# Performance work log

Measured on AMD Instinct MI355X. Metric: run time of the kernel, lower is better.

## Reference

```python
import jax, jax.numpy as jnp
import numpy as np

N_NODES = 100000


def setup_inputs() -> dict:
    key = jax.random.key(0)
    ks = jax.random.split(key, 8)
    IN, HID, OUT = 128, 128, 64
    E = 1600000
    x = jax.random.normal(ks[0], (N_NODES, IN), dtype=jnp.float32)
    edge_index = jax.random.randint(ks[1], (2, E), 0, N_NODES, dtype=jnp.int64)
    # PyG SAGEConv params: lin_l (applied to aggregated neighbors, with bias),
    # lin_r (root weight, no bias).
    def lin(k, fi, fo):
        return jax.random.normal(k, (fi, fo), dtype=jnp.float32) / np.sqrt(fi)
    Wl0 = lin(ks[2], IN, HID)
    bl0 = jnp.zeros((HID,), dtype=jnp.float32)
    Wr0 = lin(ks[3], IN, HID)
    Wl1 = lin(ks[4], HID, OUT)
    bl1 = jnp.zeros((OUT,), dtype=jnp.float32)
    Wr1 = lin(ks[5], HID, OUT)
    return {"x": x, "edge_index": edge_index,
            "Wl0": Wl0, "bl0": bl0, "Wr0": Wr0,
            "Wl1": Wl1, "bl1": bl1, "Wr1": Wr1}


def _sage_conv(h, src, dst, Wl, bl, Wr):
    # mean aggregation of source features onto target nodes
    summed = jax.ops.segment_sum(h[src], dst, num_segments=N_NODES)  # [N, d]
    cnt = jax.ops.segment_sum(jnp.ones((src.shape[0], 1), h.dtype), dst,
                              num_segments=N_NODES)                  # [N, 1]
    agg = summed / jnp.maximum(cnt, 1.0)
    return agg @ Wl + bl + h @ Wr


def reference(x, edge_index, Wl0, bl0, Wr0, Wl1, bl1, Wr1):
    src, dst = edge_index[0], edge_index[1]
    h = jax.nn.relu(_sage_conv(x, src, dst, Wl0, bl0, Wr0))
    # dropout is identity in eval mode (training=False)
    return _sage_conv(h, src, dst, Wl1, bl1, Wr1)
```

## Files before the change

### kernel.cpp

```cpp
#include <hip/hip_runtime.h>


typedef short short8 __attribute__((ext_vector_type(8)));
typedef float f32x4 __attribute__((ext_vector_type(4)));
typedef float f32x2 __attribute__((ext_vector_type(2)));

#define NBUCK 782
#define BCAP  3072
#define EPB   8192

static __device__ __forceinline__ unsigned short f2bf(float f) {
    union { float f; unsigned u; } c; c.f = f;
    unsigned u = c.u + 0x7fffu + ((c.u >> 16) & 1u);
    return (unsigned short)(u >> 16);
}
static __device__ __forceinline__ float bf2f(unsigned short b) {
    union { unsigned u; float f; } c; c.u = ((unsigned)b) << 16;
    return c.f;
}
static __device__ __forceinline__ float bf2f_s(short b) {
    return bf2f((unsigned short)b);
}

static __device__ __forceinline__ unsigned char f2fp8(float x) {
    union { float f; unsigned u; } c; c.f = x;
    unsigned s = (c.u >> 24) & 0x80u;
    float a = __builtin_fabsf(x);
    if (a < 0.015625f) {
        int m = (int)rintf(a * 512.0f);
        return (unsigned char)(s | (unsigned)m);
    }
    unsigned u = c.u + 0x7ffffu + ((c.u >> 20) & 1u);
    int e = (int)((u >> 23) & 0xff) - 120;
    unsigned m = (u >> 20) & 7u;
    if (e > 15) { e = 15; m = 6; }
    return (unsigned char)(s | (unsigned)(e << 3) | m);
}

static __device__ __forceinline__ void acc_fp8x4(unsigned w, float* a) {
#if __has_builtin(__builtin_amdgcn_cvt_pk_f32_fp8)
    f32x2 lo = __builtin_amdgcn_cvt_pk_f32_fp8((int)w, false);
    f32x2 hi = __builtin_amdgcn_cvt_pk_f32_fp8((int)w, true);
    a[0] += lo[0]; a[1] += lo[1]; a[2] += hi[0]; a[3] += hi[1];
#else
    #pragma unroll
    for (int j = 0; j < 4; ++j) {
        unsigned b = (w >> (8 * j)) & 0xffu;
        union { unsigned u; float f; } c;
        c.u = ((b & 0x80u) << 24) | ((b & 0x7fu) << 20);
        a[j] += c.f * 0x1p120f;
    }
#endif
}
static __device__ __forceinline__ void acc_row16(uint4 w, float* a) {
    acc_fp8x4(w.x, a + 0);  acc_fp8x4(w.y, a + 4);
    acc_fp8x4(w.z, a + 8);  acc_fp8x4(w.w, a + 12);
}

__global__ __launch_bounds__(256) void k_pack2(const float* __restrict__ Wl0,
        const float* __restrict__ Wr0, const float* __restrict__ Wl1,
        const float* __restrict__ Wr1, unsigned short* __restrict__ Wp0,
        unsigned short* __restrict__ Wp1) {
    int tid = blockIdx.x * 256 + threadIdx.x;
    const float *WA, *WB; int CA; unsigned short* Wp;
    if (tid < 4096) {
        WA = Wl0; WB = Wr0; CA = 128; Wp = Wp0;
    } else {
        tid -= 4096;
        if (tid >= 2048) return;
        WA = Wl1; WB = Wr1; CA = 64; Wp = Wp1;
    }
    int lane = tid & 63, kk = (tid >> 6) & 3, tg = tid >> 8;
    int l15 = lane & 15, quad = lane >> 4;
    int c = tg * 16 + l15;
    const float* W = (c < CA) ? WA : WB;
    int cc = (c < CA) ? c : c - CA;
    short8 v;
    #pragma unroll
    for (int j = 0; j < 8; ++j) {
        int k = kk * 32 + quad * 8 + j;
        v[j] = (short)f2bf(W[(size_t)k * CA + cc]);
    }
    *(short8*)(Wp + (size_t)tid * 8) = v;
}

__global__ __launch_bounds__(256) void k_gemm0_bucket(
        const float* __restrict__ X, const unsigned short* __restrict__ Wp,
        unsigned char* __restrict__ P0, unsigned short* __restrict__ Q0, int Nrows,
        const int* __restrict__ src, const int* __restrict__ dst,
        int* __restrict__ cursor, int* __restrict__ bregion,
        int E, int bucketBlocks) {
    const int t = threadIdx.x;
    if ((int)blockIdx.x >= bucketBlocks) {
        const int wave = t >> 6, lane = t & 63;
        const int quad = lane >> 4, l15 = lane & 15;
        const int row0 = (blockIdx.x - bucketBlocks) * 32;
        const int c0w = wave * 64;
        float4 xf[4][2][2];
        #pragma unroll
        for (int mt = 0; mt < 2; ++mt) {
            int row = row0 + mt * 16 + l15;
            if (row > Nrows - 1) row = Nrows - 1;
            const float* xp = X + (size_t)row * 128 + quad * 8;
            #pragma unroll
            for (int kk = 0; kk < 4; ++kk) {
                xf[kk][mt][0] = *(const float4*)(xp + kk * 32);
                xf[kk][mt][1] = *(const float4*)(xp + kk * 32 + 4);
            }
        }
        short8 a[4][2];
        #pragma unroll
        for (int kk = 0; kk < 4; ++kk)
            #pragma unroll
            for (int mt = 0; mt < 2; ++mt) {
                float4 f0 = xf[kk][mt][0], f1 = xf[kk][mt][1];
                short8 v;
                v[0] = (short)f2bf(f0.x); v[1] = (short)f2bf(f0.y);
                v[2] = (short)f2bf(f0.z); v[3] = (short)f2bf(f0.w);
                v[4] = (short)f2bf(f1.x); v[5] = (short)f2bf(f1.y);
                v[6] = (short)f2bf(f1.z); v[7] = (short)f2bf(f1.w);
                a[kk][mt] = v;
            }
        f32x4 acc[2][4];
        #pragma unroll
        for (int mt = 0; mt < 2; ++mt)
            #pragma unroll
            for (int tt = 0; tt < 4; ++tt) acc[mt][tt] = (f32x4){0.f, 0.f, 0.f, 0.f};
        #pragma unroll
        for (int kk = 0; kk < 4; ++kk) {
            short8 b[4];
            #pragma unroll
            for (int tt = 0; tt < 4; ++tt) {
                int tg = (c0w >> 4) + tt;
                b[tt] = *(const short8*)(Wp + ((size_t)(tg * 4 + kk) * 64 + lane) * 8);
            }
            #pragma unroll
            for (int mt = 0; mt < 2; ++mt)
                #pragma unroll
                for (int tt = 0; tt < 4; ++tt)
                    acc[mt][tt] = __builtin_amdgcn_mfma_f32_16x16x32_bf16(
                        a[kk][mt], b[tt], acc[mt][tt], 0, 0, 0);
        }
        #pragma unroll
        for (int mt = 0; mt < 2; ++mt)
            #pragma unroll
            for (int r = 0; r < 4; ++r) {
                int row = row0 + mt * 16 + quad * 4 + r;
                if (row < Nrows) {
                    if (c0w < 128) {
                        #pragma unroll
                        for (int tt = 0; tt < 4; ++tt)
                            P0[(size_t)row * 128 + c0w + tt * 16 + l15] =
                                f2fp8(acc[mt][tt][r]);
                    } else {
                        #pragma unroll
                        for (int tt = 0; tt < 4; ++tt)
                            Q0[(size_t)row * 128 + (c0w - 128) + tt * 16 + l15] =
                                f2bf(acc[mt][tt][r]);
                    }
                }
            }
        return;
    }
    __shared__ int hist[NBUCK];
    __shared__ int basel[NBUCK];
    int bid = blockIdx.x;
    for (int i = t; i < NBUCK; i += 256) hist[i] = 0;
    __syncthreads();
    int e0 = bid * EPB + t * 32;
    if (e0 + 32 <= E) {
        #pragma unroll
        for (int q = 0; q < 8; ++q) {
            int4 v = *(const int4*)(dst + e0 + q * 4);
            atomicAdd(&hist[v.x >> 7], 1);
            atomicAdd(&hist[v.y >> 7], 1);
            atomicAdd(&hist[v.z >> 7], 1);
            atomicAdd(&hist[v.w >> 7], 1);
        }
    } else {
        for (int j = 0; j < 32; ++j)
            if (e0 + j < E) atomicAdd(&hist[dst[e0 + j] >> 7], 1);
    }
    __syncthreads();
    for (int i = t; i < NBUCK; i += 256) {
        int c = hist[i];
        basel[i] = (c > 0) ? atomicAdd(&cursor[i], c) : 0;
    }
    __syncthreads();
    for (int i = t; i < NBUCK; i += 256) hist[i] = 0;
    __syncthreads();
    if (e0 + 32 <= E) {
        #pragma unroll
        for (int q = 0; q < 8; ++q) {
            int4 dv = *(const int4*)(dst + e0 + q * 4);
            int4 sv = *(const int4*)(src + e0 + q * 4);
            int dd[4] = {dv.x, dv.y, dv.z, dv.w};
            int ss[4] = {sv.x, sv.y, sv.z, sv.w};
            #pragma unroll
            for (int j = 0; j < 4; ++j) {
                int b = dd[j] >> 7;
                int r = atomicAdd(&hist[b], 1);
                bregion[(size_t)b * BCAP + basel[b] + r] = ss[j] | ((dd[j] & 127) << 20);
            }
        }
    } else {
        for (int j = 0; j < 32; ++j) {
            if (e0 + j < E) {
                int dd = dst[e0 + j], ss = src[e0 + j];
                int b = dd >> 7;
                int r = atomicAdd(&hist[b], 1);
                bregion[(size_t)b * BCAP + basel[b] + r] = ss | ((dd & 127) << 20);
            }
        }
    }
}

__global__ __launch_bounds__(256) void k_csr(const int* __restrict__ cursor,
                                             const int* __restrict__ bregion,
                                             int* __restrict__ rowptr,
                                             int* __restrict__ csr, int Nn) {
    __shared__ int words[BCAP];
    __shared__ int hist[128], sc[128], rank[128];
    __shared__ int red[256];
    int b = blockIdx.x, t = threadIdx.x;
    int part = 0;
    for (int i = t; i < b; i += 256) part += cursor[i];
    red[t] = part;
    if (t < 128) { hist[t] = 0; rank[t] = 0; }
    __syncthreads();
    #pragma unroll
    for (int off = 128; off > 0; off >>= 1) {
        if (t < off) red[t] += red[t + off];
        __syncthreads();
    }
    int gbase = red[0];
    int cnt = cursor[b];
    for (int i = t; i < cnt; i += 256) {
        int w = bregion[(size_t)b * BCAP + i];
        words[i] = w;
        atomicAdd(&hist[w >> 20], 1);
    }
    __syncthreads();
    if (t < 128) sc[t] = hist[t];
    __syncthreads();
    #pragma unroll
    for (int off = 1; off < 128; off <<= 1) {
        int x = 0;
        if (t < 128 && t >= off) x = sc[t - off];
        __syncthreads();
        if (t < 128) sc[t] += x;
        __syncthreads();
    }
    if (t < 128) sc[t] -= hist[t];
    __syncthreads();
    if (t < 128) {
        int node = b * 128 + t;
        if (node <= Nn) rowptr[node] = gbase + sc[t];
    }
    for (int i = t; i < cnt; i += 256) {
        int w = words[i];
        int d7 = w >> 20;
        int r = atomicAdd(&rank[d7], 1);
        csr[gbase + sc[d7] + r] = w & 0xFFFFF;
    }
}

__global__ __launch_bounds__(256) void k_agg0_gemm1(
        const unsigned char* __restrict__ P0,
        const unsigned short* __restrict__ Q0,
        const int* __restrict__ rowptr, const int* __restrict__ csr,
        const float* __restrict__ bl0,
        const unsigned short* __restrict__ Wp,
        unsigned char* __restrict__ P1, unsigned short* __restrict__ Q1,
        int Nn) {
    __shared__ unsigned short ht[32 * 128];
    const int t = threadIdx.x;
    const int wave = t >> 6, lane = t & 63;
    {
        int g = lane >> 3, l7 = lane & 7;
        int nloc = wave * 8 + g;
        int n = blockIdx.x * 32 + nloc;
        bool live = (n < Nn);
        int st = 0, dg = 0;
        if (live) { st = rowptr[n]; dg = rowptr[n + 1] - st; }
        float acc[16] = {};
        int e = 0;
        for (; e + 2 <= dg; e += 2) {
            int s0 = csr[st + e];
            int s1 = csr[st + e + 1];
            uint4 w0 = *(const uint4*)(P0 + (size_t)s0 * 128 + l7 * 16);
            uint4 w1 = *(const uint4*)(P0 + (size_t)s1 * 128 + l7 * 16);
            acc_row16(w0, acc);
            acc_row16(w1, acc);
        }
        if (e < dg) {
            int s0 = csr[st + e];
            uint4 w0 = *(const uint4*)(P0 + (size_t)s0 * 128 + l7 * 16);
            acc_row16(w0, acc);
        }
        short8 o0 = (short8){0,0,0,0,0,0,0,0}, o1 = o0;
        if (live) {
            float inv = 1.f / fmaxf((float)dg, 1.f);
            short8 q0 = *(const short8*)(Q0 + (size_t)n * 128 + l7 * 16);
            short8 q1 = *(const short8*)(Q0 + (size_t)n * 128 + l7 * 16 + 8);
            float bb[16];
            *(float4*)(bb + 0)  = *(const float4*)(bl0 + l7 * 16);
            *(float4*)(bb + 4)  = *(const float4*)(bl0 + l7 * 16 + 4);
            *(float4*)(bb + 8)  = *(const float4*)(bl0 + l7 * 16 + 8);
            *(float4*)(bb + 12) = *(const float4*)(bl0 + l7 * 16 + 12);
            #pragma unroll
            for (int j = 0; j < 8; ++j)
                o0[j] = (short)f2bf(fmaxf(acc[j] * inv + bb[j] + bf2f_s(q0[j]), 0.f));
            #pragma unroll
            for (int j = 0; j < 8; ++j)
                o1[j] = (short)f2bf(fmaxf(acc[8 + j] * inv + bb[8 + j] + bf2f_s(q1[j]), 0.f));
        }
        unsigned sw = (unsigned)(nloc & 7) << 4;
        char* base = (char*)ht + nloc * 256;
        *(short8*)(base + (((unsigned)(l7 * 32)) ^ sw)) = o0;
        *(short8*)(base + (((unsigned)(l7 * 32 + 16)) ^ sw)) = o1;
    }
    __syncthreads();
    const int quad = lane >> 4, l15 = lane & 15;
    const int row0 = blockIdx.x * 32;
    const int c0w = wave * 32;
    f32x4 acc[2][2];
    #pragma unroll
    for (int mt = 0; mt < 2; ++mt)
        #pragma unroll
        for (int tt = 0; tt < 2; ++tt) acc[mt][tt] = (f32x4){0.f, 0.f, 0.f, 0.f};
    #pragma unroll
    for (int kk = 0; kk < 4; ++kk) {
        short8 a[2];
        #pragma unroll
        for (int mt = 0; mt < 2; ++mt) {
            int row = mt * 16 + l15;
            const char* p = (const char*)ht + row * 256 +
                (((unsigned)(kk * 64 + quad * 16)) ^ ((unsigned)(row & 7) << 4));
            a[mt] = *(const short8*)p;
        }
        short8 b[2];
        #pragma unroll
        for (int tt = 0; tt < 2; ++tt) {
            int tg = (c0w >> 4) + tt;
            b[tt] = *(const short8*)(Wp + ((size_t)(tg * 4 + kk) * 64 + lane) * 8);
        }
        #pragma unroll
        for (int mt = 0; mt < 2; ++mt)
            #pragma unroll
            for (int tt = 0; tt < 2; ++tt)
                acc[mt][tt] = __builtin_amdgcn_mfma_f32_16x16x32_bf16(
                    a[mt], b[tt], acc[mt][tt], 0, 0, 0);
    }
    #pragma unroll
    for (int mt = 0; mt < 2; ++mt)
        #pragma unroll
        for (int r = 0; r < 4; ++r) {
            int row = row0 + mt * 16 + quad * 4 + r;
            if (row < Nn) {
                if (c0w < 64) {
                    #pragma unroll
                    for (int tt = 0; tt < 2; ++tt)
                        P1[(size_t)row * 64 + c0w + tt * 16 + l15] =
                            f2fp8(acc[mt][tt][r]);
                } else {
                    #pragma unroll
                    for (int tt = 0; tt < 2; ++tt)
                        Q1[(size_t)row * 64 + (c0w - 64) + tt * 16 + l15] =
                            f2bf(acc[mt][tt][r]);
                }
            }
        }
}

__global__ __launch_bounds__(256) void k_agg1(const unsigned char* __restrict__ P1,
                                              const unsigned short* __restrict__ Q1,
                                              const int* __restrict__ rowptr,
                                              const int* __restrict__ csr,
                                              const float* __restrict__ bl1,
                                              float* __restrict__ out, int Nn) {
    int wave = threadIdx.x >> 6, lane = threadIdx.x & 63;
    int g = lane >> 2, l3 = lane & 3;
    int n = (blockIdx.x * 4 + wave) * 16 + g;
    bool live = (n < Nn);
    int st = 0, dg = 0;
    if (live) { st = rowptr[n]; dg = rowptr[n + 1] - st; }
    float acc[16] = {};
    int e = 0;
    for (; e + 2 <= dg; e += 2) {
        int s0 = csr[st + e];
        int s1 = csr[st + e + 1];
        uint4 w0 = *(const uint4*)(P1 + (size_t)s0 * 64 + l3 * 16);
        uint4 w1 = *(const uint4*)(P1 + (size_t)s1 * 64 + l3 * 16);
        acc_row16(w0, acc);
        acc_row16(w1, acc);
    }
    if (e < dg) {
        int s0 = csr[st + e];
        uint4 w0 = *(const uint4*)(P1 + (size_t)s0 * 64 + l3 * 16);
        acc_row16(w0, acc);
    }
    if (live) {
        float inv = 1.f / fmaxf((float)dg, 1.f);
        short8 q0 = *(const short8*)(Q1 + (size_t)n * 64 + l3 * 16);
        short8 q1 = *(const short8*)(Q1 + (size_t)n * 64 + l3 * 16 + 8);
        float bb[16];
        *(float4*)(bb + 0)  = *(const float4*)(bl1 + l3 * 16);
        *(float4*)(bb + 4)  = *(const float4*)(bl1 + l3 * 16 + 4);
        *(float4*)(bb + 8)  = *(const float4*)(bl1 + l3 * 16 + 8);
        *(float4*)(bb + 12) = *(const float4*)(bl1 + l3 * 16 + 12);
        float4 o[4];
        #pragma unroll
        for (int j = 0; j < 8; ++j)
            ((float*)o)[j] = acc[j] * inv + bb[j] + bf2f_s(q0[j]);
        #pragma unroll
        for (int j = 0; j < 8; ++j)
            ((float*)o)[8 + j] = acc[8 + j] * inv + bb[8 + j] + bf2f_s(q1[j]);
        #pragma unroll
        for (int q = 0; q < 4; ++q)
            *(float4*)(out + (size_t)n * 64 + l3 * 16 + q * 4) = o[q];
    }
}

extern "C" void kernel_launch(void* const* d_in, const int* in_sizes, int n_in,
                              void* d_out, int out_size, void* d_ws, size_t ws_size,
                              hipStream_t stream) {
    const float* x   = (const float*)d_in[0];
    const int* eidx  = (const int*)d_in[1];
    const float* Wl0 = (const float*)d_in[2];
    const float* bl0 = (const float*)d_in[3];
    const float* Wr0 = (const float*)d_in[4];
    const float* Wl1 = (const float*)d_in[5];
    const float* bl1 = (const float*)d_in[6];
    const float* Wr1 = (const float*)d_in[7];
    float* out = (float*)d_out;

    const int N = in_sizes[0] / 128;
    const int E = in_sizes[1] / 2;
    const int* src = eidx;
    const int* dst = eidx + E;

    int* rowptr  = (int*)d_ws;
    int* cursor  = rowptr + (N + 4);
    int* bregion = cursor + 784;
    int* csr     = bregion + (size_t)NBUCK * BCAP;
    unsigned short* Wp0 = (unsigned short*)(csr + E);
    unsigned short* Wp1 = Wp0 + 32768;
    unsigned char*  P0  = (unsigned char*)(Wp1 + 16384);
    unsigned short* Q0  = (unsigned short*)(P0 + (size_t)N * 128);
    unsigned char*  P1  = (unsigned char*)(Q0 + (size_t)N * 128);
    unsigned short* Q1  = (unsigned short*)(P1 + (size_t)N * 64);

    hipMemsetAsync(cursor, 0, NBUCK * sizeof(int), stream);

    k_pack2<<<24, 256, 0, stream>>>(Wl0, Wr0, Wl1, Wr1, Wp0, Wp1);

    int gemmBlocks = (N + 31) / 32;
    int nbb = (E + EPB - 1) / EPB;
    k_gemm0_bucket<<<gemmBlocks + nbb, 256, 0, stream>>>(
        x, Wp0, P0, Q0, N, src, dst, cursor, bregion, E, nbb);
    k_csr<<<NBUCK, 256, 0, stream>>>(cursor, bregion, rowptr, csr, N);

    k_agg0_gemm1<<<(N + 31) / 32, 256, 0, stream>>>(
        P0, Q0, rowptr, csr, bl0, Wp1, P1, Q1, N);
    k_agg1<<<(N + 63) / 64, 256, 0, stream>>>(P1, Q1, rowptr, csr, bl1, out, N);
}
```

Measured before the change: 278.6 us.

## Split bucket and gemm0 kernels; stage bucketed edges in LDS for coalesced writes

The fused gemm0+bucket kernel is split into two separate launches, k_bucket and k_gemm0. The bucketing kernel now scans the per-block histogram to sort its edges locally in shared memory, then writes them to the bucket regions in bucket order rather than scattering single words. This aims to make global writes contiguous per bucket. In exchange, the bucket kernel uses much more LDS (about 56KB), which lowers its occupancy, and it adds an extra launch plus a serialized stage that can no longer overlap with the GEMM blocks.

```diff
diff --git a/kernel.cpp b/kernel.cpp
--- a/kernel.cpp
+++ b/kernel.cpp
@@ -84,87 +84,17 @@
     *(short8*)(Wp + (size_t)tid * 8) = v;
 }
 
-__global__ __launch_bounds__(256) void k_gemm0_bucket(
-        const float* __restrict__ X, const unsigned short* __restrict__ Wp,
-        unsigned char* __restrict__ P0, unsigned short* __restrict__ Q0, int Nrows,
+__global__ __launch_bounds__(256) void k_bucket(
         const int* __restrict__ src, const int* __restrict__ dst,
-        int* __restrict__ cursor, int* __restrict__ bregion,
-        int E, int bucketBlocks) {
+        int* __restrict__ cursor, int* __restrict__ bregion, int E) {
+    __shared__ int hist[NBUCK];
+    __shared__ int obase[NBUCK];
+    __shared__ int basel[NBUCK];
+    __shared__ int stagedw[EPB];
+    __shared__ unsigned short stagedb[EPB];
+    __shared__ int scanred[256];
     const int t = threadIdx.x;
-    if ((int)blockIdx.x >= bucketBlocks) {
-        const int wave = t >> 6, lane = t & 63;
-        const int quad = lane >> 4, l15 = lane & 15;
-        const int row0 = (blockIdx.x - bucketBlocks) * 32;
-        const int c0w = wave * 64;
-        float4 xf[4][2][2];
-        #pragma unroll
-        for (int mt = 0; mt < 2; ++mt) {
-            int row = row0 + mt * 16 + l15;
-            if (row > Nrows - 1) row = Nrows - 1;
-            const float* xp = X + (size_t)row * 128 + quad * 8;
-            #pragma unroll
-            for (int kk = 0; kk < 4; ++kk) {
-                xf[kk][mt][0] = *(const float4*)(xp + kk * 32);
-                xf[kk][mt][1] = *(const float4*)(xp + kk * 32 + 4);
-            }
-        }
-        short8 a[4][2];
-        #pragma unroll
-        for (int kk = 0; kk < 4; ++kk)
-            #pragma unroll
-            for (int mt = 0; mt < 2; ++mt) {
-                float4 f0 = xf[kk][mt][0], f1 = xf[kk][mt][1];
-                short8 v;
-                v[0] = (short)f2bf(f0.x); v[1] = (short)f2bf(f0.y);
-                v[2] = (short)f2bf(f0.z); v[3] = (short)f2bf(f0.w);
-                v[4] = (short)f2bf(f1.x); v[5] = (short)f2bf(f1.y);
-                v[6] = (short)f2bf(f1.z); v[7] = (short)f2bf(f1.w);
-                a[kk][mt] = v;
-            }
-        f32x4 acc[2][4];
-        #pragma unroll
-        for (int mt = 0; mt < 2; ++mt)
-            #pragma unroll
-            for (int tt = 0; tt < 4; ++tt) acc[mt][tt] = (f32x4){0.f, 0.f, 0.f, 0.f};
-        #pragma unroll
-        for (int kk = 0; kk < 4; ++kk) {
-            short8 b[4];
-            #pragma unroll
-            for (int tt = 0; tt < 4; ++tt) {
-                int tg = (c0w >> 4) + tt;
-                b[tt] = *(const short8*)(Wp + ((size_t)(tg * 4 + kk) * 64 + lane) * 8);
-            }
-            #pragma unroll
-            for (int mt = 0; mt < 2; ++mt)
-                #pragma unroll
-                for (int tt = 0; tt < 4; ++tt)
-                    acc[mt][tt] = __builtin_amdgcn_mfma_f32_16x16x32_bf16(
-                        a[kk][mt], b[tt], acc[mt][tt], 0, 0, 0);
-        }
-        #pragma unroll
-        for (int mt = 0; mt < 2; ++mt)
-            #pragma unroll
-            for (int r = 0; r < 4; ++r) {
-                int row = row0 + mt * 16 + quad * 4 + r;
-                if (row < Nrows) {
-                    if (c0w < 128) {
-                        #pragma unroll
-                        for (int tt = 0; tt < 4; ++tt)
-                            P0[(size_t)row * 128 + c0w + tt * 16 + l15] =
-                                f2fp8(acc[mt][tt][r]);
-                    } else {
-                        #pragma unroll
-                        for (int tt = 0; tt < 4; ++tt)
-                            Q0[(size_t)row * 128 + (c0w - 128) + tt * 16 + l15] =
-                                f2bf(acc[mt][tt][r]);
-                    }
-                }
-            }
-        return;
-    }
-    __shared__ int hist[NBUCK];
-    __shared__ int basel[NBUCK];
-    int bid = blockIdx.x;
+    const int bid = blockIdx.x;
     for (int i = t; i < NBUCK; i += 256) hist[i] = 0;
     __syncthreads();
     int e0 = bid * EPB + t * 32;
@@ -182,10 +112,30 @@
             if (e0 + j < E) atomicAdd(&hist[dst[e0 + j] >> 7], 1);
     }
     __syncthreads();
-    for (int i = t; i < NBUCK; i += 256) {
-        int c = hist[i];
-        basel[i] = (c > 0) ? atomicAdd(&cursor[i], c) : 0;
-    }
+    int i0 = t * 4;
+    int h0 = (i0 + 0 < NBUCK) ? hist[i0 + 0] : 0;
+    int h1 = (i0 + 1 < NBUCK) ? hist[i0 + 1] : 0;
+    int h2 = (i0 + 2 < NBUCK) ? hist[i0 + 2] : 0;
+    int h3 = (i0 + 3 < NBUCK) ? hist[i0 + 3] : 0;
+    int lsum = h0 + h1 + h2 + h3;
+    scanred[t] = lsum;
+    __syncthreads();
+    #pragma unroll
+    for (int off = 1; off < 256; off <<= 1) {
+        int x = (t >= off) ? scanred[t - off] : 0;
+        __syncthreads();
+        scanred[t] += x;
+        __syncthreads();
+    }
+    int excl = scanred[t] - lsum;
+    if (i0 + 0 < NBUCK) obase[i0 + 0] = excl;
+    if (i0 + 1 < NBUCK) obase[i0 + 1] = excl + h0;
+    if (i0 + 2 < NBUCK) obase[i0 + 2] = excl + h0 + h1;
+    if (i0 + 3 < NBUCK) obase[i0 + 3] = excl + h0 + h1 + h2;
+    if (i0 + 0 < NBUCK) basel[i0 + 0] = h0 ? atomicAdd(&cursor[i0 + 0], h0) : 0;
+    if (i0 + 1 < NBUCK) basel[i0 + 1] = h1 ? atomicAdd(&cursor[i0 + 1], h1) : 0;
+    if (i0 + 2 < NBUCK) basel[i0 + 2] = h2 ? atomicAdd(&cursor[i0 + 2], h2) : 0;
+    if (i0 + 3 < NBUCK) basel[i0 + 3] = h3 ? atomicAdd(&cursor[i0 + 3], h3) : 0;
     __syncthreads();
     for (int i = t; i < NBUCK; i += 256) hist[i] = 0;
     __syncthreads();
@@ -200,7 +150,9 @@
             for (int j = 0; j < 4; ++j) {
                 int b = dd[j] >> 7;
                 int r = atomicAdd(&hist[b], 1);
-                bregion[(size_t)b * BCAP + basel[b] + r] = ss[j] | ((dd[j] & 127) << 20);
+                int slot = obase[b] + r;
+                stagedw[slot] = ss[j] | ((dd[j] & 127) << 20);
+                stagedb[slot] = (unsigned short)b;
             }
         }
     } else {
@@ -209,10 +161,94 @@
                 int dd = dst[e0 + j], ss = src[e0 + j];
                 int b = dd >> 7;
                 int r = atomicAdd(&hist[b], 1);
-                bregion[(size_t)b * BCAP + basel[b] + r] = ss | ((dd & 127) << 20);
+                int slot = obase[b] + r;
+                stagedw[slot] = ss | ((dd & 127) << 20);
+                stagedb[slot] = (unsigned short)b;
             }
         }
     }
+    __syncthreads();
+    int tot = E - bid * EPB; if (tot > EPB) tot = EPB;
+    for (int i = t; i < tot; i += 256) {
+        int w = stagedw[i];
+        int b = stagedb[i];
+        bregion[(size_t)b * BCAP + basel[b] + (i - obase[b])] = w;
+    }
+}
+
+__global__ __launch_bounds__(256) void k_gemm0(
+        const float* __restrict__ X, const unsigned short* __restrict__ Wp,
+        unsigned char* __restrict__ P0, unsigned short* __restrict__ Q0,
+        int Nrows) {
+    const int t = threadIdx.x;
+    const int wave = t >> 6, lane = t & 63;
+    const int quad = lane >> 4, l15 = lane & 15;
+    const int row0 = blockIdx.x * 32;
+    const int c0w = wave * 64;
+    float4 xf[4][2][2];
+    #pragma unroll
+    for (int mt = 0; mt < 2; ++mt) {
+        int row = row0 + mt * 16 + l15;
+        if (row > Nrows - 1) row = Nrows - 1;
+        const float* xp = X + (size_t)row * 128 + quad * 8;
+        #pragma unroll
+        for (int kk = 0; kk < 4; ++kk) {
+            xf[kk][mt][0] = *(const float4*)(xp + kk * 32);
+            xf[kk][mt][1] = *(const float4*)(xp + kk * 32 + 4);
+        }
+    }
+    short8 a[4][2];
+    #pragma unroll
+    for (int kk = 0; kk < 4; ++kk)
+        #pragma unroll
+        for (int mt = 0; mt < 2; ++mt) {
+            float4 f0 = xf[kk][mt][0], f1 = xf[kk][mt][1];
+            short8 v;
+            v[0] = (short)f2bf(f0.x); v[1] = (short)f2bf(f0.y);
+            v[2] = (short)f2bf(f0.z); v[3] = (short)f2bf(f0.w);
+            v[4] = (short)f2bf(f1.x); v[5] = (short)f2bf(f1.y);
+            v[6] = (short)f2bf(f1.z); v[7] = (short)f2bf(f1.w);
+            a[kk][mt] = v;
+        }
+    f32x4 acc[2][4];
+    #pragma unroll
+    for (int mt = 0; mt < 2; ++mt)
+        #pragma unroll
+        for (int tt = 0; tt < 4; ++tt) acc[mt][tt] = (f32x4){0.f, 0.f, 0.f, 0.f};
+    #pragma unroll
+    for (int kk = 0; kk < 4; ++kk) {
+        short8 b[4];
+        #pragma unroll
+        for (int tt = 0; tt < 4; ++tt) {
+            int tg = (c0w >> 4) + tt;
+            b[tt] = *(const short8*)(Wp + ((size_t)(tg * 4 + kk) * 64 + lane) * 8);
+        }
+        #pragma unroll
+        for (int mt = 0; mt < 2; ++mt)
+            #pragma unroll
+            for (int tt = 0; tt < 4; ++tt)
+                acc[mt][tt] = __builtin_amdgcn_mfma_f32_16x16x32_bf16(
+                    a[kk][mt], b[tt], acc[mt][tt], 0, 0, 0);
+    }
+    #pragma unroll
+    for (int mt = 0; mt < 2; ++mt)
+        #pragma unroll
+        for (int r = 0; r < 4; ++r) {
+            int row = row0 + mt * 16 + quad * 4 + r;
+            if (row < Nrows) {
+                if (c0w < 128) {
+                    #pragma unroll
+                    for (int tt = 0; tt < 4; ++tt)
+                        P0[(size_t)row * 128 + c0w + tt * 16 + l15] =
+                            f2fp8(acc[mt][tt][r]);
+                } else {
+                    #pragma unroll
+                    for (int tt = 0; tt < 4; ++tt)
+                        Q0[(size_t)row * 128 + (c0w - 128) + tt * 16 + l15] =
+                            f2bf(acc[mt][tt][r]);
+                }
+            }
+        }
 }
 
 __global__ __launch_bounds__(256) void k_csr(const int* __restrict__ cursor,
@@ -455,10 +491,9 @@
 
     k_pack2<<<24, 256, 0, stream>>>(Wl0, Wr0, Wl1, Wr1, Wp0, Wp1);
 
-    int gemmBlocks = (N + 31) / 32;
     int nbb = (E + EPB - 1) / EPB;
-    k_gemm0_bucket<<<gemmBlocks + nbb, 256, 0, stream>>>(
-        x, Wp0, P0, Q0, N, src, dst, cursor, bregion, E, nbb);
+    k_bucket<<<nbb, 256, 0, stream>>>(src, dst, cursor, bregion, E);
+    k_gemm0<<<(N + 31) / 32, 256, 0, stream>>>(x, Wp0, P0, Q0, N);
     k_csr<<<NBUCK, 256, 0, stream>>>(cursor, bregion, rowptr, csr, N);
 
     k_agg0_gemm1<<<(N + 31) / 32, 256, 0, stream>>>(
```

Measured after the change: 294.7 us. 5.8% more time.

## Balance neighbor aggregation by splitting block edge ranges evenly across lanes

Applied to the files above, without the earlier changes.

Both aggregation kernels now split the contiguous CSR edge range of a node block evenly across lane groups, instead of giving each group one node's edges. Each CSR word keeps the local destination index in its high bits, so a group can tell when it crosses a node boundary and flush its partial sums into a shared-memory accumulator with atomics. The goal is to remove load imbalance and divergence from uneven node degrees, and to software-pipeline the next row gather. The cost is extra LDS atomics, zero-initialisation and additional barriers.

```diff
diff --git a/kernel.cpp b/kernel.cpp
--- a/kernel.cpp
+++ b/kernel.cpp
@@ -261,7 +261,7 @@
         int w = words[i];
         int d7 = w >> 20;
         int r = atomicAdd(&rank[d7], 1);
-        csr[gbase + sc[d7] + r] = w & 0xFFFFF;
+        csr[gbase + sc[d7] + r] = w;
     }
 }
 
@@ -273,34 +273,66 @@
         const unsigned short* __restrict__ Wp,
         unsigned char* __restrict__ P1, unsigned short* __restrict__ Q1,
         int Nn) {
+    __shared__ float accs[32 * 128];
     __shared__ unsigned short ht[32 * 128];
     const int t = threadIdx.x;
     const int wave = t >> 6, lane = t & 63;
+    const int n0 = blockIdx.x * 32;
     {
-        int g = lane >> 3, l7 = lane & 7;
-        int nloc = wave * 8 + g;
-        int n = blockIdx.x * 32 + nloc;
-        bool live = (n < Nn);
-        int st = 0, dg = 0;
-        if (live) { st = rowptr[n]; dg = rowptr[n + 1] - st; }
-        float acc[16] = {};
-        int e = 0;
-        for (; e + 2 <= dg; e += 2) {
-            int s0 = csr[st + e];
-            int s1 = csr[st + e + 1];
-            uint4 w0 = *(const uint4*)(P0 + (size_t)s0 * 128 + l7 * 16);
-            uint4 w1 = *(const uint4*)(P0 + (size_t)s1 * 128 + l7 * 16);
-            acc_row16(w0, acc);
-            acc_row16(w1, acc);
-        }
-        if (e < dg) {
-            int s0 = csr[st + e];
-            uint4 w0 = *(const uint4*)(P0 + (size_t)s0 * 128 + l7 * 16);
-            acc_row16(w0, acc);
-        }
+        int l7 = lane & 7;
+        int g = wave * 8 + (lane >> 3);
+        for (int i2 = t; i2 < 32 * 128; i2 += 256) accs[i2] = 0.f;
+        __syncthreads();
+        int st0 = rowptr[n0];
+        int en  = rowptr[n0 + 32];
+        int T = en - st0;
+        int q = (T + 31) >> 5;
+        int gbeg = st0 + g * q; if (gbeg > en) gbeg = en;
+        int gend = gbeg + q;    if (gend > en) gend = en;
+        float a[16];
+        #pragma unroll
+        for (int j = 0; j < 16; ++j) a[j] = 0.f;
+        int cur = -1;
+        int i = gbeg;
+        int wcur = 0; uint4 rcur = (uint4){0, 0, 0, 0};
+        if (i < gend) {
+            wcur = csr[i];
+            rcur = *(const uint4*)(P0 + (size_t)(wcur & 0xFFFFF) * 128 + l7 * 16);
+        }
+        while (i < gend) {
+            int wnext = 0; uint4 rnext = rcur;
+            if (i + 1 < gend) {
+                wnext = csr[i + 1];
+                rnext = *(const uint4*)(P0 + (size_t)(wnext & 0xFFFFF) * 128 + l7 * 16);
+            }
+            int loc = (wcur >> 20) & 31;
+            if (loc != cur) {
+                if (cur >= 0) {
+                    #pragma unroll
+                    for (int j = 0; j < 16; ++j)
+                        atomicAdd(&accs[cur * 128 + l7 * 16 + j], a[j]);
+                    #pragma unroll
+                    for (int j = 0; j < 16; ++j) a[j] = 0.f;
+                }
+                cur = loc;
+            }
+            acc_row16(rcur, a);
+            wcur = wnext; rcur = rnext; ++i;
+        }
+        if (cur >= 0) {
+            #pragma unroll
+            for (int j = 0; j < 16; ++j)
+                atomicAdd(&accs[cur * 128 + l7 * 16 + j], a[j]);
+        }
+        __syncthreads();
+        int n = n0 + g;
         short8 o0 = (short8){0,0,0,0,0,0,0,0}, o1 = o0;
-        if (live) {
-            float inv = 1.f / fmaxf((float)dg, 1.f);
+        if (n < Nn) {
+            int dgr = rowptr[n + 1] - rowptr[n];
+            float inv = 1.f / fmaxf((float)dgr, 1.f);
+            float va[16];
+            #pragma unroll
+            for (int j = 0; j < 16; ++j) va[j] = accs[g * 128 + l7 * 16 + j];
             short8 q0 = *(const short8*)(Q0 + (size_t)n * 128 + l7 * 16);
             short8 q1 = *(const short8*)(Q0 + (size_t)n * 128 + l7 * 16 + 8);
             float bb[16];
@@ -310,13 +342,13 @@
             *(float4*)(bb + 12) = *(const float4*)(bl0 + l7 * 16 + 12);
             #pragma unroll
             for (int j = 0; j < 8; ++j)
-                o0[j] = (short)f2bf(fmaxf(acc[j] * inv + bb[j] + bf2f_s(q0[j]), 0.f));
+                o0[j] = (short)f2bf(fmaxf(va[j] * inv + bb[j] + bf2f_s(q0[j]), 0.f));
             #pragma unroll
             for (int j = 0; j < 8; ++j)
-                o1[j] = (short)f2bf(fmaxf(acc[8 + j] * inv + bb[8 + j] + bf2f_s(q1[j]), 0.f));
-        }
-        unsigned sw = (unsigned)(nloc & 7) << 4;
-        char* base = (char*)ht + nloc * 256;
+                o1[j] = (short)f2bf(fmaxf(va[8 + j] * inv + bb[8 + j] + bf2f_s(q1[j]), 0.f));
+        }
+        unsigned sw = (unsigned)(g & 7) << 4;
+        char* base = (char*)ht + g * 256;
         *(short8*)(base + (((unsigned)(l7 * 32)) ^ sw)) = o0;
         *(short8*)(base + (((unsigned)(l7 * 32 + 16)) ^ sw)) = o1;
     }
@@ -379,29 +411,64 @@
                                               const int* __restrict__ csr,
                                               const float* __restrict__ bl1,
                                               float* __restrict__ out, int Nn) {
-    int wave = threadIdx.x >> 6, lane = threadIdx.x & 63;
-    int g = lane >> 2, l3 = lane & 3;
-    int n = (blockIdx.x * 4 + wave) * 16 + g;
-    bool live = (n < Nn);
-    int st = 0, dg = 0;
-    if (live) { st = rowptr[n]; dg = rowptr[n + 1] - st; }
-    float acc[16] = {};
-    int e = 0;
-    for (; e + 2 <= dg; e += 2) {
-        int s0 = csr[st + e];
-        int s1 = csr[st + e + 1];
-        uint4 w0 = *(const uint4*)(P1 + (size_t)s0 * 64 + l3 * 16);
-        uint4 w1 = *(const uint4*)(P1 + (size_t)s1 * 64 + l3 * 16);
-        acc_row16(w0, acc);
-        acc_row16(w1, acc);
-    }
-    if (e < dg) {
-        int s0 = csr[st + e];
-        uint4 w0 = *(const uint4*)(P1 + (size_t)s0 * 64 + l3 * 16);
-        acc_row16(w0, acc);
-    }
-    if (live) {
-        float inv = 1.f / fmaxf((float)dg, 1.f);
+    __shared__ float accs[64 * 64];
+    const int t = threadIdx.x;
+    const int wave = t >> 6, lane = t & 63;
+    const int l3 = lane & 3;
+    const int g = wave * 16 + (lane >> 2);
+    const int n0 = blockIdx.x * 64;
+    int nvalid = Nn - n0; if (nvalid > 64) nvalid = 64;
+    for (int i2 = t; i2 < 64 * 64; i2 += 256) accs[i2] = 0.f;
+    __syncthreads();
+    int st0 = rowptr[n0];
+    int en  = rowptr[n0 + nvalid];
+    int T = en - st0;
+    int q = (T + 63) >> 6;
+    int gbeg = st0 + g * q; if (gbeg > en) gbeg = en;
+    int gend = gbeg + q;    if (gend > en) gend = en;
+    float a[16];
+    #pragma unroll
+    for (int j = 0; j < 16; ++j) a[j] = 0.f;
+    int cur = -1;
+    int i = gbeg;
+    int wcur = 0; uint4 rcur = (uint4){0, 0, 0, 0};
+    if (i < gend) {
+        wcur = csr[i];
+        rcur = *(const uint4*)(P1 + (size_t)(wcur & 0xFFFFF) * 64 + l3 * 16);
+    }
+    while (i < gend) {
+        int wnext = 0; uint4 rnext = rcur;
+        if (i + 1 < gend) {
+            wnext = csr[i + 1];
+            rnext = *(const uint4*)(P1 + (size_t)(wnext & 0xFFFFF) * 64 + l3 * 16);
+        }
+        int loc = (wcur >> 20) & 63;
+        if (loc != cur) {
+            if (cur >= 0) {
+                #pragma unroll
+                for (int j = 0; j < 16; ++j)
+                    atomicAdd(&accs[cur * 64 + l3 * 16 + j], a[j]);
+                #pragma unroll
+                for (int j = 0; j < 16; ++j) a[j] = 0.f;
+            }
+            cur = loc;
+        }
+        acc_row16(rcur, a);
+        wcur = wnext; rcur = rnext; ++i;
+    }
+    if (cur >= 0) {
+        #pragma unroll
+        for (int j = 0; j < 16; ++j)
+            atomicAdd(&accs[cur * 64 + l3 * 16 + j], a[j]);
+    }
+    __syncthreads();
+    int n = n0 + g;
+    if (n < Nn) {
+        int dgr = rowptr[n + 1] - rowptr[n];
+        float inv = 1.f / fmaxf((float)dgr, 1.f);
+        float va[16];
+        #pragma unroll
+        for (int j = 0; j < 16; ++j) va[j] = accs[g * 64 + l3 * 16 + j];
         short8 q0 = *(const short8*)(Q1 + (size_t)n * 64 + l3 * 16);
         short8 q1 = *(const short8*)(Q1 + (size_t)n * 64 + l3 * 16 + 8);
         float bb[16];
@@ -412,13 +479,13 @@
         float4 o[4];
         #pragma unroll
         for (int j = 0; j < 8; ++j)
-            ((float*)o)[j] = acc[j] * inv + bb[j] + bf2f_s(q0[j]);
+            ((float*)o)[j] = va[j] * inv + bb[j] + bf2f_s(q0[j]);
         #pragma unroll
         for (int j = 0; j < 8; ++j)
-            ((float*)o)[8 + j] = acc[8 + j] * inv + bb[8 + j] + bf2f_s(q1[j]);
-        #pragma unroll
-        for (int q = 0; q < 4; ++q)
-            *(float4*)(out + (size_t)n * 64 + l3 * 16 + q * 4) = o[q];
+            ((float*)o)[8 + j] = va[8 + j] * inv + bb[8 + j] + bf2f_s(q1[j]);
+        #pragma unroll
+        for (int qq = 0; qq < 4; ++qq)
+            *(float4*)(out + (size_t)n * 64 + l3 * 16 + qq * 4) = o[qq];
     }
 }
 
```

Result: slower. 406.6 us (+45.9%).
